# Performance work log

Measured on AMD Instinct MI355X. Metric: run time of the kernel, lower is better.

## Reference

```python
import jax, jax.numpy as jnp
import numpy as np

H = 4096      # hidden_size (Llama-7B)
I = 11008     # intermediate_size (Llama-7B)
T = 4096      # tokens = batch 2 * seq 2048


def setup_inputs() -> dict:
    key = jax.random.key(0)
    ks = jax.random.split(key, 10)
    # int8 activations in [-128, 127]
    x = jax.random.randint(ks[0], (T, H), -128, 128, dtype=jnp.int32).astype(jnp.int8)
    # int4 weights stored as int8 values in [-8, 7], layout [out, in]
    gate_w = jax.random.randint(ks[1], (I, H), -8, 8, dtype=jnp.int32).astype(jnp.int8)
    up_w   = jax.random.randint(ks[2], (I, H), -8, 8, dtype=jnp.int32).astype(jnp.int8)
    down_w = jax.random.randint(ks[3], (H, I), -8, 8, dtype=jnp.int32).astype(jnp.int8)
    # per-output-channel dequant scale (input_scale * weight_scale) and fp32 bias
    gate_alpha = jax.random.uniform(ks[4], (I,), jnp.float32, 1e-4, 3e-4)
    up_alpha   = jax.random.uniform(ks[5], (I,), jnp.float32, 1e-4, 3e-4)
    down_alpha = jax.random.uniform(ks[6], (H,), jnp.float32, 1e-4, 3e-4)
    gate_bias = jax.random.normal(ks[7], (I,), jnp.float32) * 0.01
    up_bias   = jax.random.normal(ks[8], (I,), jnp.float32) * 0.01
    down_bias = jax.random.normal(ks[9], (H,), jnp.float32) * 0.01
    down_input_scale = jnp.array(0.1, dtype=jnp.float32)
    return dict(x=x, gate_w=gate_w, up_w=up_w, down_w=down_w,
                gate_alpha=gate_alpha, gate_bias=gate_bias,
                up_alpha=up_alpha, up_bias=up_bias,
                down_alpha=down_alpha, down_bias=down_bias,
                down_input_scale=down_input_scale)


def _w4a8_linear(x_i8, w_i4, alpha, bias):
    # int8 act x int4 weight -> int32 accumulate, per-out-channel dequant, fp32 out
    acc = jnp.matmul(x_i8.astype(jnp.int32), w_i4.T.astype(jnp.int32))  # [T, out]
    return acc.astype(jnp.float32) * alpha + bias


def reference(x, gate_w, up_w, down_w, gate_alpha, gate_bias, up_alpha, up_bias,
              down_alpha, down_bias, down_input_scale):
    g = _w4a8_linear(x, gate_w, gate_alpha, gate_bias)          # [T, I] fp32
    u = _w4a8_linear(x, up_w, up_alpha, up_bias)                # [T, I] fp32
    h = jax.nn.silu(g) * u                                      # SwiGLU
    # requantize to int8 for down_proj input (values kept exact as fp32)
    hq = jnp.clip(jnp.round(h / down_input_scale), -128.0, 127.0)
    out = jnp.matmul(hq, down_w.T.astype(jnp.float32)) * down_alpha + down_bias
    return out
```

## Files before the change

kernel.cpp:

```cpp
#include <hip/hip_runtime.h>
#include <stdint.h>

#define H_DIM 4096
#define I_DIM 11008
#define T_DIM 4096

typedef int i32x4 __attribute__((ext_vector_type(4)));
typedef const void __attribute__((address_space(1))) gvoid_t;
typedef void __attribute__((address_space(3))) svoid_t;

__device__ __forceinline__ void gload_lds16(const void* gsrc, void* ldst) {
    __builtin_amdgcn_global_load_lds((gvoid_t*)gsrc, (svoid_t*)ldst, 16, 0, 0);
}
__device__ __forceinline__ void wait_vmcnt5() {
    asm volatile("s_waitcnt vmcnt(5)" ::: "memory");
}
__device__ __forceinline__ void wait_vmcnt0() {
    asm volatile("s_waitcnt vmcnt(0)" ::: "memory");
}
__device__ __forceinline__ void wait_lgkm0() {
    asm volatile("s_waitcnt lgkmcnt(0)" ::: "memory");
    __builtin_amdgcn_sched_barrier(0);
}
__device__ __forceinline__ void barrier_() {
    asm volatile("s_barrier" ::: "memory");
}

__device__ __forceinline__ uint32_t pack4(int4 v) {
    uint32_t r = (uint32_t)(uint8_t)v.x;
    r |= (uint32_t)(uint8_t)v.y << 8;
    r |= (uint32_t)(uint8_t)v.z << 16;
    r |= (uint32_t)(uint8_t)v.w << 24;
    return r;
}

__global__ void convert_kernel(const int* __restrict__ src, int8_t* __restrict__ dst,
                               int n4) {
    int idx = blockIdx.x * blockDim.x + threadIdx.x;
    int stride = gridDim.x * blockDim.x;
    for (int i = idx; i < n4; i += stride) {
        int4 v = ((const int4*)src)[i];
        ((uint32_t*)dst)[i] = pack4(v);
    }
}

__global__ void convert_frag_kernel(const int* __restrict__ src, int8_t* __restrict__ dst,
                                    int nslots, int kdiv16) {
    const int K = kdiv16 << 4;
    int idx = blockIdx.x * blockDim.x + threadIdx.x;
    int stride = gridDim.x * blockDim.x;
    for (int s = idx; s < nslots; s += stride) {
        const int n_lo = s & 15;
        const int srem = s >> 4;
        const int ks = srem % kdiv16;
        const int nb = srem / kdiv16;
        const int4* p = (const int4*)(src + (size_t)(nb * 16 + n_lo) * K + ks * 16);
        uint4 w;
        w.x = pack4(p[0]); w.y = pack4(p[1]); w.z = pack4(p[2]); w.w = pack4(p[3]);
        const size_t doff = ((size_t)nb * (kdiv16 >> 2) + (ks >> 2)) * 1024
                          + (size_t)(ks & 3) * 256 + (size_t)n_lo * 16;
        *(uint4*)(dst + doff) = w;
    }
}

#define MFMA_I8 __builtin_amdgcn_mfma_i32_16x16x64_i8

__global__ __launch_bounds__(512, 4)
void gateup_kernel(const int8_t* __restrict__ x8, const int8_t* __restrict__ gwf,
                   const int8_t* __restrict__ uwf,
                   const float* __restrict__ galpha, const float* __restrict__ gbias,
                   const float* __restrict__ ualpha, const float* __restrict__ ubias,
                   const float* __restrict__ scale_p, int8_t* __restrict__ hq)
{
    __shared__ __align__(16) int8_t smem_s[32768];
    int8_t* lsA = smem_s;

    const int bid = blockIdx.x;
    const int mt = bid & 31;
    const int nt = bid >> 5;
    const int m0 = mt << 7;
    const int n0 = nt << 7;

    const int tid  = threadIdx.x;
    const int lane = tid & 63;
    const int wid  = tid >> 6;
    const int isU  = wid >> 2;
    const int w4   = wid & 3;
    const int wr   = w4 >> 1;
    const int wc   = w4 & 1;
    const int lr   = lane & 15;
    const int rdsw = ((lane >> 4) ^ ((lr >> 1) & 3)) << 4;

    const int srow = tid >> 2;
    const int scol = ((tid & 3) ^ ((tid >> 3) & 3)) << 4;
    const int woff = wid << 10;

    const int8_t* As = x8 + (size_t)(m0 + srow) * H_DIM + scol;
    const int KB64 = H_DIM >> 6;
    const int8_t* Bsel = isU ? uwf : gwf;
    const int8_t* Bq = Bsel + ((size_t)((n0 >> 4) + wc * 4) * KB64) * 1024 + lane * 16;

    i32x4 acc[4][4];
#pragma unroll
    for (int mf = 0; mf < 4; ++mf)
#pragma unroll
        for (int nf = 0; nf < 4; ++nf) acc[mf][nf] = i32x4{0, 0, 0, 0};

    const int aro = (wr * 64 + lr) * 64 + rdsw;

#define STAGE_A(b, kb) gload_lds16(As + (kb), lsA + (b) * 8192 + woff)
#define BLOAD(BF, tt) do { \
        _Pragma("unroll") for (int nf = 0; nf < 4; ++nf) \
            BF[nf] = *(const i32x4*)(Bq + ((size_t)nf * KB64 + (tt)) * 1024); \
    } while (0)

#define ITER_GU(tt, BF, BFN) do { \
        wait_vmcnt5(); \
        barrier_(); \
        i32x4 af[4]; \
        _Pragma("unroll") for (int mf = 0; mf < 4; ++mf) \
            af[mf] = *(const i32x4*)(lsA + ((tt) & 1) * 8192 + aro + mf * 1024); \
        wait_lgkm0(); \
        barrier_(); \
        BLOAD(BFN, (((tt) + 1) & (NKT - 1))); \
        STAGE_A((tt) & 1, (((tt) + 2) & (NKT - 1)) << 6); \
        _Pragma("unroll") for (int mf = 0; mf < 4; ++mf) \
        _Pragma("unroll") for (int nf = 0; nf < 4; ++nf) \
            acc[mf][nf] = MFMA_I8(af[mf], BF[nf], acc[mf][nf], 0, 0, 0); \
    } while (0)

    const int NKT = H_DIM / 64;
    i32x4 bfA[4], bfB[4];
    STAGE_A(0, 0);
    BLOAD(bfA, 0);
    STAGE_A(1, 64);

    for (int t = 0; t < NKT; t += 2) {
        ITER_GU(t, bfA, bfB);
        ITER_GU(t + 1, bfB, bfA);
    }
#undef ITER_GU
#undef BLOAD
#undef STAGE_A
    wait_vmcnt0();
    barrier_();

    const float scale = *scale_p;
#pragma unroll
    for (int h = 0; h < 2; ++h) {
        if (isU) {
#pragma unroll
            for (int mf = 0; mf < 4; ++mf)
#pragma unroll
                for (int q = 0; q < 2; ++q)
                    *(i32x4*)(smem_s + w4 * 8192 + mf * 2048 + q * 1024 + lane * 16)
                        = acc[mf][h * 2 + q];
        }
        barrier_();
        if (!isU) {
#pragma unroll
            for (int q = 0; q < 2; ++q) {
                const int nf = h * 2 + q;
                const int col = n0 + wc * 64 + nf * 16 + lr;
                const float gA = galpha[col], gB = gbias[col];
                const float uA = ualpha[col], uB = ubias[col];
#pragma unroll
                for (int mf = 0; mf < 4; ++mf) {
                    i32x4 uacc = *(const i32x4*)(smem_s + w4 * 8192 + mf * 2048
                                                 + q * 1024 + lane * 16);
                    const int row0 = m0 + wr * 64 + mf * 16 + (lane >> 4) * 4;
#pragma unroll
                    for (int j = 0; j < 4; ++j) {
                        float g = (float)acc[mf][nf][j] * gA + gB;
                        float u = (float)uacc[j] * uA + uB;
                        float s = 1.0f / (1.0f + __expf(-g));
                        float hh = g * s * u;
                        float qv = rintf(hh / scale);
                        qv = fminf(127.0f, fmaxf(-128.0f, qv));
                        hq[(size_t)(row0 + j) * I_DIM + col] = (int8_t)qv;
                    }
                }
            }
        }
        barrier_();
    }
}

__global__ __launch_bounds__(512, 4)
void down_kernel(const int8_t* __restrict__ hq, const int8_t* __restrict__ dwf,
                 const float* __restrict__ dalpha, const float* __restrict__ dbias,
                 float* __restrict__ out)
{
    __shared__ __align__(16) int8_t smem_d[16384];
    int8_t* lsA = smem_d;

    const int bid = blockIdx.x;
    const int mt = bid & 31;
    const int nt = bid >> 5;
    const int m0 = mt << 7;
    const int n0 = nt << 8;

    const int tid  = threadIdx.x;
    const int lane = tid & 63;
    const int wid  = tid >> 6;
    const int wr   = wid >> 2;
    const int wc   = wid & 3;
    const int lr   = lane & 15;
    const int rdsw = ((lane >> 4) ^ ((lr >> 1) & 3)) << 4;

    const int srow = tid >> 2;
    const int scol = ((tid & 3) ^ ((tid >> 3) & 3)) << 4;
    const int woff = wid << 10;

    const int8_t* Ap = hq + (size_t)(m0 + srow) * I_DIM + scol;
    const int KB64 = I_DIM >> 6;
    const int8_t* Bq = dwf + ((size_t)((n0 >> 4) + wc * 4) * KB64) * 1024 + lane * 16;

    i32x4 acc[4][4];
#pragma unroll
    for (int mf = 0; mf < 4; ++mf)
#pragma unroll
        for (int nf = 0; nf < 4; ++nf) acc[mf][nf] = i32x4{0, 0, 0, 0};

    const int aro = (wr * 64 + lr) * 64 + rdsw;

#define STAGE_A(b, kb) gload_lds16(Ap + (kb), lsA + (b) * 8192 + woff)
#define BLOAD(BF, tt) do { \
        _Pragma("unroll") for (int nf = 0; nf < 4; ++nf) \
            BF[nf] = *(const i32x4*)(Bq + ((size_t)nf * KB64 + (tt)) * 1024); \
    } while (0)

#define ITER_D(tt, BF, BFN) do { \
        wait_vmcnt5(); \
        barrier_(); \
        i32x4 af[4]; \
        _Pragma("unroll") for (int mf = 0; mf < 4; ++mf) \
            af[mf] = *(const i32x4*)(lsA + ((tt) & 1) * 8192 + aro + mf * 1024); \
        wait_lgkm0(); \
        barrier_(); \
        BLOAD(BFN, ((tt) + 1) % NKT); \
        STAGE_A((tt) & 1, (size_t)((((tt) + 2) % NKT) * 64)); \
        _Pragma("unroll") for (int mf = 0; mf < 4; ++mf) \
        _Pragma("unroll") for (int nf = 0; nf < 4; ++nf) \
            acc[mf][nf] = MFMA_I8(af[mf], BF[nf], acc[mf][nf], 0, 0, 0); \
    } while (0)

    const int NKT = I_DIM / 64;
    i32x4 bfA[4], bfB[4];
    STAGE_A(0, 0);
    BLOAD(bfA, 0);
    STAGE_A(1, 64);

    for (int t = 0; t < NKT; t += 2) {
        ITER_D(t, bfA, bfB);
        ITER_D(t + 1, bfB, bfA);
    }
#undef ITER_D
#undef BLOAD
#undef STAGE_A
    wait_vmcnt0();

#pragma unroll
    for (int nf = 0; nf < 4; ++nf) {
        const int col = n0 + wc * 64 + nf * 16 + lr;
        const float dA = dalpha[col], dB = dbias[col];
#pragma unroll
        for (int mf = 0; mf < 4; ++mf) {
            const int row0 = m0 + wr * 64 + mf * 16 + (lane >> 4) * 4;
#pragma unroll
            for (int j = 0; j < 4; ++j) {
                out[(size_t)(row0 + j) * H_DIM + col] = (float)acc[mf][nf][j] * dA + dB;
            }
        }
    }
}

extern "C" void kernel_launch(void* const* d_in, const int* in_sizes, int n_in,
                              void* d_out, int out_size, void* d_ws, size_t ws_size,
                              hipStream_t stream) {
    const int* x32  = (const int*)d_in[0];
    const int* gw32 = (const int*)d_in[1];
    const int* uw32 = (const int*)d_in[2];
    const int* dw32 = (const int*)d_in[3];
    const float* ga = (const float*)d_in[4];
    const float* gb = (const float*)d_in[5];
    const float* ua = (const float*)d_in[6];
    const float* ub = (const float*)d_in[7];
    const float* da = (const float*)d_in[8];
    const float* db = (const float*)d_in[9];
    const float* sc = (const float*)d_in[10];
    float* out = (float*)d_out;

    const size_t SZ_X8 = (size_t)T_DIM * H_DIM;
    const size_t SZ_W  = (size_t)I_DIM * H_DIM;
    const size_t SZ_HQ = (size_t)T_DIM * I_DIM;

    int8_t* gwf = (int8_t*)d_ws;
    int8_t* uwf = gwf + SZ_W;
    int8_t* hq  = uwf + SZ_W;
    int8_t* x8  = hq + SZ_HQ;

    convert_kernel<<<dim3(2048), dim3(256), 0, stream>>>(x32, x8, (int)(SZ_X8 / 4));
    convert_frag_kernel<<<dim3(2048), dim3(256), 0, stream>>>(
        gw32, gwf, (int)(SZ_W / 16), H_DIM / 16);
    convert_frag_kernel<<<dim3(2048), dim3(256), 0, stream>>>(
        uw32, uwf, (int)(SZ_W / 16), H_DIM / 16);
    gateup_kernel<<<dim3(32 * 86), dim3(512), 0, stream>>>(
        x8, gwf, uwf, ga, gb, ua, ub, sc, hq);
    int8_t* dwf = gwf;
    convert_frag_kernel<<<dim3(2048), dim3(256), 0, stream>>>(
        dw32, dwf, (int)(SZ_W / 16), I_DIM / 16);
    down_kernel<<<dim3(32 * 16), dim3(512), 0, stream>>>(hq, dwf, da, db, out);
}
```

Baseline: 703.7 us.

## Load A operands directly from global in MFMA fragment layout, drop LDS staging

Both GEMM kernels now read the activation operand straight from global memory into registers, using a pre-permuted fragment layout. The input x is reformatted by convert_frag_kernel, and the gate/up epilogue writes hq directly in that fragment layout. This removes the LDS staging, swizzles and the two barriers per k-step, and wraps the MFMA blocks in s_setprio. In exchange, each wave loads A fragments redundantly from global/L2 with no LDS sharing, hq stores become scattered byte writes, and launch bounds drop to 3 waves per SIMD.

```diff
diff --git a/kernel.cpp b/kernel.cpp
--- a/kernel.cpp
+++ b/kernel.cpp
@@ -6,25 +6,6 @@
 #define T_DIM 4096
 
 typedef int i32x4 __attribute__((ext_vector_type(4)));
-typedef const void __attribute__((address_space(1))) gvoid_t;
-typedef void __attribute__((address_space(3))) svoid_t;
-
-__device__ __forceinline__ void gload_lds16(const void* gsrc, void* ldst) {
-    __builtin_amdgcn_global_load_lds((gvoid_t*)gsrc, (svoid_t*)ldst, 16, 0, 0);
-}
-__device__ __forceinline__ void wait_vmcnt5() {
-    asm volatile("s_waitcnt vmcnt(5)" ::: "memory");
-}
-__device__ __forceinline__ void wait_vmcnt0() {
-    asm volatile("s_waitcnt vmcnt(0)" ::: "memory");
-}
-__device__ __forceinline__ void wait_lgkm0() {
-    asm volatile("s_waitcnt lgkmcnt(0)" ::: "memory");
-    __builtin_amdgcn_sched_barrier(0);
-}
-__device__ __forceinline__ void barrier_() {
-    asm volatile("s_barrier" ::: "memory");
-}
 
 __device__ __forceinline__ uint32_t pack4(int4 v) {
     uint32_t r = (uint32_t)(uint8_t)v.x;
@@ -32,16 +13,6 @@
     r |= (uint32_t)(uint8_t)v.z << 16;
     r |= (uint32_t)(uint8_t)v.w << 24;
     return r;
-}
-
-__global__ void convert_kernel(const int* __restrict__ src, int8_t* __restrict__ dst,
-                               int n4) {
-    int idx = blockIdx.x * blockDim.x + threadIdx.x;
-    int stride = gridDim.x * blockDim.x;
-    for (int i = idx; i < n4; i += stride) {
-        int4 v = ((const int4*)src)[i];
-        ((uint32_t*)dst)[i] = pack4(v);
-    }
 }
 
 __global__ void convert_frag_kernel(const int* __restrict__ src, int8_t* __restrict__ dst,
@@ -65,15 +36,14 @@
 
 #define MFMA_I8 __builtin_amdgcn_mfma_i32_16x16x64_i8
 
-__global__ __launch_bounds__(512, 4)
-void gateup_kernel(const int8_t* __restrict__ x8, const int8_t* __restrict__ gwf,
+__global__ __launch_bounds__(512, 3)
+void gateup_kernel(const int8_t* __restrict__ x8f, const int8_t* __restrict__ gwf,
                    const int8_t* __restrict__ uwf,
                    const float* __restrict__ galpha, const float* __restrict__ gbias,
                    const float* __restrict__ ualpha, const float* __restrict__ ubias,
-                   const float* __restrict__ scale_p, int8_t* __restrict__ hq)
+                   const float* __restrict__ scale_p, int8_t* __restrict__ hqf)
 {
     __shared__ __align__(16) int8_t smem_s[32768];
-    int8_t* lsA = smem_s;
 
     const int bid = blockIdx.x;
     const int mt = bid & 31;
@@ -89,14 +59,9 @@
     const int wr   = w4 >> 1;
     const int wc   = w4 & 1;
     const int lr   = lane & 15;
-    const int rdsw = ((lane >> 4) ^ ((lr >> 1) & 3)) << 4;
-
-    const int srow = tid >> 2;
-    const int scol = ((tid & 3) ^ ((tid >> 3) & 3)) << 4;
-    const int woff = wid << 10;
-
-    const int8_t* As = x8 + (size_t)(m0 + srow) * H_DIM + scol;
+
     const int KB64 = H_DIM >> 6;
+    const int8_t* Aq = x8f + ((size_t)((m0 >> 4) + wr * 4) * KB64) * 1024 + lane * 16;
     const int8_t* Bsel = isU ? uwf : gwf;
     const int8_t* Bq = Bsel + ((size_t)((n0 >> 4) + wc * 4) * KB64) * 1024 + lane * 16;
 
@@ -106,46 +71,39 @@
 #pragma unroll
         for (int nf = 0; nf < 4; ++nf) acc[mf][nf] = i32x4{0, 0, 0, 0};
 
-    const int aro = (wr * 64 + lr) * 64 + rdsw;
-
-#define STAGE_A(b, kb) gload_lds16(As + (kb), lsA + (b) * 8192 + woff)
-#define BLOAD(BF, tt) do { \
+#define LOADF(AF, BF, tt) do { \
+        _Pragma("unroll") for (int mf = 0; mf < 4; ++mf) \
+            AF[mf] = *(const i32x4*)(Aq + ((size_t)mf * KB64 + (tt)) * 1024); \
         _Pragma("unroll") for (int nf = 0; nf < 4; ++nf) \
             BF[nf] = *(const i32x4*)(Bq + ((size_t)nf * KB64 + (tt)) * 1024); \
     } while (0)
 
-#define ITER_GU(tt, BF, BFN) do { \
-        wait_vmcnt5(); \
-        barrier_(); \
-        i32x4 af[4]; \
-        _Pragma("unroll") for (int mf = 0; mf < 4; ++mf) \
-            af[mf] = *(const i32x4*)(lsA + ((tt) & 1) * 8192 + aro + mf * 1024); \
-        wait_lgkm0(); \
-        barrier_(); \
-        BLOAD(BFN, (((tt) + 1) & (NKT - 1))); \
-        STAGE_A((tt) & 1, (((tt) + 2) & (NKT - 1)) << 6); \
-        _Pragma("unroll") for (int mf = 0; mf < 4; ++mf) \
-        _Pragma("unroll") for (int nf = 0; nf < 4; ++nf) \
-            acc[mf][nf] = MFMA_I8(af[mf], BF[nf], acc[mf][nf], 0, 0, 0); \
+#define MFMA16(AF, BF) do { \
+        __builtin_amdgcn_s_setprio(1); \
+        _Pragma("unroll") for (int mf = 0; mf < 4; ++mf) \
+        _Pragma("unroll") for (int nf = 0; nf < 4; ++nf) \
+            acc[mf][nf] = MFMA_I8(AF[mf], BF[nf], acc[mf][nf], 0, 0, 0); \
+        __builtin_amdgcn_s_setprio(0); \
     } while (0)
 
     const int NKT = H_DIM / 64;
-    i32x4 bfA[4], bfB[4];
-    STAGE_A(0, 0);
-    BLOAD(bfA, 0);
-    STAGE_A(1, 64);
-
+    i32x4 aA[4], bA[4], aB[4], bB[4];
+    LOADF(aA, bA, 0);
     for (int t = 0; t < NKT; t += 2) {
-        ITER_GU(t, bfA, bfB);
-        ITER_GU(t + 1, bfB, bfA);
-    }
-#undef ITER_GU
-#undef BLOAD
-#undef STAGE_A
-    wait_vmcnt0();
-    barrier_();
+        LOADF(aB, bB, (t + 1) & (NKT - 1));
+        MFMA16(aA, bA);
+        LOADF(aA, bA, (t + 2) & (NKT - 1));
+        MFMA16(aB, bB);
+    }
+#undef LOADF
+#undef MFMA16
+
+    __syncthreads();
 
     const float scale = *scale_p;
+    const int KBI = I_DIM >> 6;
+    const int rtile0 = (m0 >> 4) + wr * 4;
+    const int kblk = (n0 + wc * 64) >> 6;
 #pragma unroll
     for (int h = 0; h < 2; ++h) {
         if (isU) {
@@ -156,7 +114,7 @@
                     *(i32x4*)(smem_s + w4 * 8192 + mf * 2048 + q * 1024 + lane * 16)
                         = acc[mf][h * 2 + q];
         }
-        barrier_();
+        __syncthreads();
         if (!isU) {
 #pragma unroll
             for (int q = 0; q < 2; ++q) {
@@ -168,7 +126,8 @@
                 for (int mf = 0; mf < 4; ++mf) {
                     i32x4 uacc = *(const i32x4*)(smem_s + w4 * 8192 + mf * 2048
                                                  + q * 1024 + lane * 16);
-                    const int row0 = m0 + wr * 64 + mf * 16 + (lane >> 4) * 4;
+                    int8_t* hb = hqf + ((size_t)(rtile0 + mf) * KBI + kblk) * 1024
+                               + nf * 256 + lr;
 #pragma unroll
                     for (int j = 0; j < 4; ++j) {
                         float g = (float)acc[mf][nf][j] * gA + gB;
@@ -177,23 +136,20 @@
                         float hh = g * s * u;
                         float qv = rintf(hh / scale);
                         qv = fminf(127.0f, fmaxf(-128.0f, qv));
-                        hq[(size_t)(row0 + j) * I_DIM + col] = (int8_t)qv;
+                        hb[((lane >> 4) * 4 + j) * 16] = (int8_t)qv;
                     }
                 }
             }
         }
-        barrier_();
-    }
-}
-
-__global__ __launch_bounds__(512, 4)
-void down_kernel(const int8_t* __restrict__ hq, const int8_t* __restrict__ dwf,
+        __syncthreads();
+    }
+}
+
+__global__ __launch_bounds__(512, 3)
+void down_kernel(const int8_t* __restrict__ hqf, const int8_t* __restrict__ dwf,
                  const float* __restrict__ dalpha, const float* __restrict__ dbias,
                  float* __restrict__ out)
 {
-    __shared__ __align__(16) int8_t smem_d[16384];
-    int8_t* lsA = smem_d;
-
     const int bid = blockIdx.x;
     const int mt = bid & 31;
     const int nt = bid >> 5;
@@ -206,14 +162,9 @@
     const int wr   = wid >> 2;
     const int wc   = wid & 3;
     const int lr   = lane & 15;
-    const int rdsw = ((lane >> 4) ^ ((lr >> 1) & 3)) << 4;
-
-    const int srow = tid >> 2;
-    const int scol = ((tid & 3) ^ ((tid >> 3) & 3)) << 4;
-    const int woff = wid << 10;
-
-    const int8_t* Ap = hq + (size_t)(m0 + srow) * I_DIM + scol;
+
     const int KB64 = I_DIM >> 6;
+    const int8_t* Aq = hqf + ((size_t)((m0 >> 4) + wr * 4) * KB64) * 1024 + lane * 16;
     const int8_t* Bq = dwf + ((size_t)((n0 >> 4) + wc * 4) * KB64) * 1024 + lane * 16;
 
     i32x4 acc[4][4];
@@ -222,43 +173,32 @@
 #pragma unroll
         for (int nf = 0; nf < 4; ++nf) acc[mf][nf] = i32x4{0, 0, 0, 0};
 
-    const int aro = (wr * 64 + lr) * 64 + rdsw;
-
-#define STAGE_A(b, kb) gload_lds16(Ap + (kb), lsA + (b) * 8192 + woff)
-#define BLOAD(BF, tt) do { \
+#define LOADF(AF, BF, tt) do { \
+        _Pragma("unroll") for (int mf = 0; mf < 4; ++mf) \
+            AF[mf] = *(const i32x4*)(Aq + ((size_t)mf * KB64 + (tt)) * 1024); \
         _Pragma("unroll") for (int nf = 0; nf < 4; ++nf) \
             BF[nf] = *(const i32x4*)(Bq + ((size_t)nf * KB64 + (tt)) * 1024); \
     } while (0)
 
-#define ITER_D(tt, BF, BFN) do { \
-        wait_vmcnt5(); \
-        barrier_(); \
-        i32x4 af[4]; \
-        _Pragma("unroll") for (int mf = 0; mf < 4; ++mf) \
-            af[mf] = *(const i32x4*)(lsA + ((tt) & 1) * 8192 + aro + mf * 1024); \
-        wait_lgkm0(); \
-        barrier_(); \
-        BLOAD(BFN, ((tt) + 1) % NKT); \
-        STAGE_A((tt) & 1, (size_t)((((tt) + 2) % NKT) * 64)); \
-        _Pragma("unroll") for (int mf = 0; mf < 4; ++mf) \
-        _Pragma("unroll") for (int nf = 0; nf < 4; ++nf) \
-            acc[mf][nf] = MFMA_I8(af[mf], BF[nf], acc[mf][nf], 0, 0, 0); \
+#define MFMA16(AF, BF) do { \
+        __builtin_amdgcn_s_setprio(1); \
+        _Pragma("unroll") for (int mf = 0; mf < 4; ++mf) \
+        _Pragma("unroll") for (int nf = 0; nf < 4; ++nf) \
+            acc[mf][nf] = MFMA_I8(AF[mf], BF[nf], acc[mf][nf], 0, 0, 0); \
+        __builtin_amdgcn_s_setprio(0); \
     } while (0)
 
     const int NKT = I_DIM / 64;
-    i32x4 bfA[4], bfB[4];
-    STAGE_A(0, 0);
-    BLOAD(bfA, 0);
-    STAGE_A(1, 64);
-
+    i32x4 aA[4], bA[4], aB[4], bB[4];
+    LOADF(aA, bA, 0);
     for (int t = 0; t < NKT; t += 2) {
-        ITER_D(t, bfA, bfB);
-        ITER_D(t + 1, bfB, bfA);
-    }
-#undef ITER_D
-#undef BLOAD
-#undef STAGE_A
-    wait_vmcnt0();
+        LOADF(aB, bB, (t + 1) % NKT);
+        MFMA16(aA, bA);
+        LOADF(aA, bA, (t + 2) % NKT);
+        MFMA16(aB, bB);
+    }
+#undef LOADF
+#undef MFMA16
 
 #pragma unroll
     for (int nf = 0; nf < 4; ++nf) {
@@ -297,18 +237,19 @@
 
     int8_t* gwf = (int8_t*)d_ws;
     int8_t* uwf = gwf + SZ_W;
-    int8_t* hq  = uwf + SZ_W;
-    int8_t* x8  = hq + SZ_HQ;
-
-    convert_kernel<<<dim3(2048), dim3(256), 0, stream>>>(x32, x8, (int)(SZ_X8 / 4));
+    int8_t* hqf = uwf + SZ_W;
+    int8_t* x8f = hqf + SZ_HQ;
+
+    convert_frag_kernel<<<dim3(2048), dim3(256), 0, stream>>>(
+        x32, x8f, (int)(SZ_X8 / 16), H_DIM / 16);
     convert_frag_kernel<<<dim3(2048), dim3(256), 0, stream>>>(
         gw32, gwf, (int)(SZ_W / 16), H_DIM / 16);
     convert_frag_kernel<<<dim3(2048), dim3(256), 0, stream>>>(
         uw32, uwf, (int)(SZ_W / 16), H_DIM / 16);
     gateup_kernel<<<dim3(32 * 86), dim3(512), 0, stream>>>(
-        x8, gwf, uwf, ga, gb, ua, ub, sc, hq);
+        x8f, gwf, uwf, ga, gb, ua, ub, sc, hqf);
     int8_t* dwf = gwf;
     convert_frag_kernel<<<dim3(2048), dim3(256), 0, stream>>>(
         dw32, dwf, (int)(SZ_W / 16), I_DIM / 16);
-    down_kernel<<<dim3(32 * 16), dim3(512), 0, stream>>>(hq, dwf, da, db, out);
-}
+    down_kernel<<<dim3(32 * 16), dim3(512), 0, stream>>>(hqf, dwf, da, db, out);
+}
```

New measurement: 863.7 us. +22.7%, slower.

## Stage activation tiles in four-k-tile chunks to cut barriers per K step

Applied to the files above, without the earlier changes.

Both GEMM kernels now load the activation (A) operand into LDS in chunks of four 64-wide k-tiles, double-buffered as 2×32KB. Each chunk is consumed by four inner MFMA steps under a single wait/barrier pair, where before every k-tile had two barriers. The aim is to spend less time on synchronisation and issue per K step. In exchange each block now needs 64KB of LDS, which likely caps resident blocks per CU below the launch-bound target of 4. The vmcnt threshold is also raised to 8 to match the larger chunked loads.

```diff
diff --git a/kernel.cpp b/kernel.cpp
--- a/kernel.cpp
+++ b/kernel.cpp
@@ -12,8 +12,8 @@
 __device__ __forceinline__ void gload_lds16(const void* gsrc, void* ldst) {
     __builtin_amdgcn_global_load_lds((gvoid_t*)gsrc, (svoid_t*)ldst, 16, 0, 0);
 }
-__device__ __forceinline__ void wait_vmcnt5() {
-    asm volatile("s_waitcnt vmcnt(5)" ::: "memory");
+__device__ __forceinline__ void wait_vmcnt8() {
+    asm volatile("s_waitcnt vmcnt(8)" ::: "memory");
 }
 __device__ __forceinline__ void wait_vmcnt0() {
     asm volatile("s_waitcnt vmcnt(0)" ::: "memory");
@@ -72,8 +72,7 @@
                    const float* __restrict__ ualpha, const float* __restrict__ ubias,
                    const float* __restrict__ scale_p, int8_t* __restrict__ hq)
 {
-    __shared__ __align__(16) int8_t smem_s[32768];
-    int8_t* lsA = smem_s;
+    __shared__ __align__(16) int8_t smem_s[65536];
 
     const int bid = blockIdx.x;
     const int mt = bid & 31;
@@ -108,40 +107,49 @@
 
     const int aro = (wr * 64 + lr) * 64 + rdsw;
 
-#define STAGE_A(b, kb) gload_lds16(As + (kb), lsA + (b) * 8192 + woff)
+#define STAGE_CH(b, ch) do { \
+        _Pragma("unroll") for (int i_ = 0; i_ < 4; ++i_) \
+            gload_lds16(As + (ch) * 256 + i_ * 64, \
+                        smem_s + (b) * 32768 + i_ * 8192 + woff); \
+    } while (0)
+
 #define BLOAD(BF, tt) do { \
         _Pragma("unroll") for (int nf = 0; nf < 4; ++nf) \
             BF[nf] = *(const i32x4*)(Bq + ((size_t)nf * KB64 + (tt)) * 1024); \
     } while (0)
 
-#define ITER_GU(tt, BF, BFN) do { \
-        wait_vmcnt5(); \
-        barrier_(); \
+#define INNER(i_, BF, BFN, c_) do { \
         i32x4 af[4]; \
         _Pragma("unroll") for (int mf = 0; mf < 4; ++mf) \
-            af[mf] = *(const i32x4*)(lsA + ((tt) & 1) * 8192 + aro + mf * 1024); \
-        wait_lgkm0(); \
-        barrier_(); \
-        BLOAD(BFN, (((tt) + 1) & (NKT - 1))); \
-        STAGE_A((tt) & 1, (((tt) + 2) & (NKT - 1)) << 6); \
+            af[mf] = *(const i32x4*)(smem_s + ((c_) & 1) * 32768 + (i_) * 8192 \
+                                     + aro + mf * 1024); \
+        BLOAD(BFN, ((c_) * 4 + (i_) + 1) & (NKT - 1)); \
         _Pragma("unroll") for (int mf = 0; mf < 4; ++mf) \
         _Pragma("unroll") for (int nf = 0; nf < 4; ++nf) \
             acc[mf][nf] = MFMA_I8(af[mf], BF[nf], acc[mf][nf], 0, 0, 0); \
     } while (0)
 
     const int NKT = H_DIM / 64;
+    const int NC  = NKT / 4;
     i32x4 bfA[4], bfB[4];
-    STAGE_A(0, 0);
+    STAGE_CH(0, 0);
+    STAGE_CH(1, 1);
     BLOAD(bfA, 0);
-    STAGE_A(1, 64);
-
-    for (int t = 0; t < NKT; t += 2) {
-        ITER_GU(t, bfA, bfB);
-        ITER_GU(t + 1, bfB, bfA);
-    }
-#undef ITER_GU
+
+    for (int c = 0; c < NC; ++c) {
+        wait_vmcnt8();
+        barrier_();
+        INNER(0, bfA, bfB, c);
+        INNER(1, bfB, bfA, c);
+        INNER(2, bfA, bfB, c);
+        INNER(3, bfB, bfA, c);
+        wait_lgkm0();
+        barrier_();
+        STAGE_CH(c & 1, (c + 2) & (NC - 1));
+    }
+#undef INNER
 #undef BLOAD
-#undef STAGE_A
+#undef STAGE_CH
     wait_vmcnt0();
     barrier_();
 
@@ -191,8 +199,7 @@
                  const float* __restrict__ dalpha, const float* __restrict__ dbias,
                  float* __restrict__ out)
 {
-    __shared__ __align__(16) int8_t smem_d[16384];
-    int8_t* lsA = smem_d;
+    __shared__ __align__(16) int8_t smem_d[65536];
 
     const int bid = blockIdx.x;
     const int mt = bid & 31;
@@ -224,40 +231,49 @@
 
     const int aro = (wr * 64 + lr) * 64 + rdsw;
 
-#define STAGE_A(b, kb) gload_lds16(Ap + (kb), lsA + (b) * 8192 + woff)
+#define STAGE_CH(b, ch) do { \
+        _Pragma("unroll") for (int i_ = 0; i_ < 4; ++i_) \
+            gload_lds16(Ap + (size_t)(ch) * 256 + i_ * 64, \
+                        smem_d + (b) * 32768 + i_ * 8192 + woff); \
+    } while (0)
+
 #define BLOAD(BF, tt) do { \
         _Pragma("unroll") for (int nf = 0; nf < 4; ++nf) \
             BF[nf] = *(const i32x4*)(Bq + ((size_t)nf * KB64 + (tt)) * 1024); \
     } while (0)
 
-#define ITER_D(tt, BF, BFN) do { \
-        wait_vmcnt5(); \
-        barrier_(); \
+#define INNER(i_, BF, BFN, c_) do { \
         i32x4 af[4]; \
         _Pragma("unroll") for (int mf = 0; mf < 4; ++mf) \
-            af[mf] = *(const i32x4*)(lsA + ((tt) & 1) * 8192 + aro + mf * 1024); \
-        wait_lgkm0(); \
-        barrier_(); \
-        BLOAD(BFN, ((tt) + 1) % NKT); \
-        STAGE_A((tt) & 1, (size_t)((((tt) + 2) % NKT) * 64)); \
+            af[mf] = *(const i32x4*)(smem_d + ((c_) & 1) * 32768 + (i_) * 8192 \
+                                     + aro + mf * 1024); \
+        BLOAD(BFN, ((c_) * 4 + (i_) + 1) % NKT); \
         _Pragma("unroll") for (int mf = 0; mf < 4; ++mf) \
         _Pragma("unroll") for (int nf = 0; nf < 4; ++nf) \
             acc[mf][nf] = MFMA_I8(af[mf], BF[nf], acc[mf][nf], 0, 0, 0); \
     } while (0)
 
     const int NKT = I_DIM / 64;
+    const int NC  = NKT / 4;
     i32x4 bfA[4], bfB[4];
-    STAGE_A(0, 0);
+    STAGE_CH(0, 0);
+    STAGE_CH(1, 1);
     BLOAD(bfA, 0);
-    STAGE_A(1, 64);
-
-    for (int t = 0; t < NKT; t += 2) {
-        ITER_D(t, bfA, bfB);
-        ITER_D(t + 1, bfB, bfA);
-    }
-#undef ITER_D
+
+    for (int c = 0; c < NC; ++c) {
+        wait_vmcnt8();
+        barrier_();
+        INNER(0, bfA, bfB, c);
+        INNER(1, bfB, bfA, c);
+        INNER(2, bfA, bfB, c);
+        INNER(3, bfB, bfA, c);
+        wait_lgkm0();
+        barrier_();
+        STAGE_CH(c & 1, (c + 2) % NC);
+    }
+#undef INNER
 #undef BLOAD
-#undef STAGE_A
+#undef STAGE_CH
     wait_vmcnt0();
 
 #pragma unroll
```

After: 702.6 us. Within noise of the previous version (-0.2%).
